# Kernel optimization log

Measured on AMD Instinct MI355X. Metric: run time of the kernel, lower is better.

## Reference

```python
import jax, jax.numpy as jnp
import numpy as np

B, S, D, H = 2, 2048, 1024, 16
DK = D // H
NEG = -65504.0  # matches torch masked_fill value in source


def setup_inputs() -> dict:
    key = jax.random.key(0)
    ks = jax.random.split(key, 5)
    scale = 1.0 / np.sqrt(D)
    return {
        "x": jax.random.normal(ks[0], (B, S, D), dtype=jnp.float32),
        "W_q": jax.random.normal(ks[1], (D, D), dtype=jnp.float32) * scale,
        "W_k": jax.random.normal(ks[2], (D, D), dtype=jnp.float32) * scale,
        "W_v": jax.random.normal(ks[3], (D, D), dtype=jnp.float32) * scale,
        "W_o": jax.random.normal(ks[4], (D, D), dtype=jnp.float32) * scale,
    }


def reference(x, W_q, W_k, W_v, W_o):
    b, s, d = x.shape
    # nn.Linear(x) = x @ W.T ; split heads -> [b, h, s, dk]
    def proj(W):
        return (x @ W.T).reshape(b, s, H, DK).transpose(0, 2, 1, 3)
    q, k, v = proj(W_q), proj(W_k), proj(W_v)
    scores = jnp.einsum("bhqd,bhkd->bhqk", q, k) / jnp.sqrt(jnp.float32(DK))
    causal = jnp.tril(jnp.ones((s, s), dtype=bool))  # True where attending allowed
    scores = jnp.where(causal, scores, NEG)
    attn = jax.nn.softmax(scores, axis=-1)  # attn_pdrop=0 -> dropout is identity
    out = jnp.einsum("bhqk,bhkd->bhqd", attn, v)
    out = out.transpose(0, 2, 1, 3).reshape(b, s, d)
    return out @ W_o.T
```

## Files before the change

### kernel.cpp

```cpp
#include <hip/hip_runtime.h>
#include <hip/hip_bf16.h>

typedef __attribute__((ext_vector_type(4))) float f32x4;
typedef __attribute__((ext_vector_type(8))) short bf16x8;

#define Bn 2
#define Sn 2048
#define Dn 1024
#define Hn 16
#define DKn 64
#define Mrows (Bn * Sn)

__device__ __forceinline__ unsigned short f2bf(float f) {
  unsigned int x = __float_as_uint(f);
  x += 0x7fffu + ((x >> 16) & 1u);
  return (unsigned short)(x >> 16);
}

__device__ __forceinline__ float bf2f(unsigned short u) {
  return __uint_as_float(((unsigned int)u) << 16);
}

__device__ __forceinline__ unsigned int cvtpk(float lo, float hi) {
  unsigned int r;
  asm("v_cvt_pk_bf16_f32 %0, %1, %2" : "=v"(r) : "v"(lo), "v"(hi));
  return r;
}

__device__ __forceinline__ float exp2a(float x) {
  float r;
  asm("v_exp_f32 %0, %1" : "=v"(r) : "v"(x));
  return r;
}

__device__ __forceinline__ f32x4 mfma16(bf16x8 a, bf16x8 b, f32x4 c) {
  return __builtin_amdgcn_mfma_f32_16x16x32_bf16(a, b, c, 0, 0, 0);
}

__device__ __forceinline__ f32x4 max4(f32x4 a, f32x4 b) {
  f32x4 r;
  r[0] = fmaxf(a[0], b[0]); r[1] = fmaxf(a[1], b[1]);
  r[2] = fmaxf(a[2], b[2]); r[3] = fmaxf(a[3], b[3]);
  return r;
}

__device__ __forceinline__ void gload_lds16(const unsigned short* g, unsigned short* l) {
  __builtin_amdgcn_global_load_lds(
      (const __attribute__((address_space(1))) void*)g,
      (__attribute__((address_space(3))) void*)l, 16, 0, 0);
}

__global__ __launch_bounds__(256)
void cvt_all(const float* __restrict__ x,  const float* __restrict__ wq,
             const float* __restrict__ wk, const float* __restrict__ wv,
             const float* __restrict__ wo,
             unsigned short* __restrict__ xb,  unsigned short* __restrict__ wqb,
             unsigned short* __restrict__ wkb, unsigned short* __restrict__ wvb,
             unsigned short* __restrict__ wob) {
  int i = (blockIdx.x * 256 + threadIdx.x) * 4;
  const float* src; unsigned short* dst; int off;
  int r = i >> 20;
  if (r < 4)       { src = x;  dst = xb;  off = i; }
  else if (r == 4) { src = wq; dst = wqb; off = i & 1048575; }
  else if (r == 5) { src = wk; dst = wkb; off = i & 1048575; }
  else if (r == 6) { src = wv; dst = wvb; off = i & 1048575; }
  else             { src = wo; dst = wob; off = i & 1048575; }
  float4 v = *(const float4*)(src + off);
  ushort4 o;
  o.x = f2bf(v.x); o.y = f2bf(v.y); o.z = f2bf(v.z); o.w = f2bf(v.w);
  *(ushort4*)(dst + off) = o;
}

template<int MODE>
__device__ __forceinline__ void gemm_body(const unsigned short* __restrict__ A,
                                          const unsigned short* __restrict__ W,
                                          unsigned short* __restrict__ Cb,
                                          float* __restrict__ Cf,
                                          unsigned short* As,
                                          unsigned short* Bs,
                                          int row0, int col0) {
  const int K = Dn, N = Dn;
  const int tid  = threadIdx.x;
  const int wid  = tid >> 6;
  const int lane = tid & 63;
  const int l15  = lane & 15;
  const int lg   = lane >> 4;
  const int wr = (wid >> 1) * 64;
  const int wc = (wid & 1) * 64;

  f32x4 acc[4][4] = {};

  const int lrow2 = lane >> 2;
  const int gs    = (lane & 3) ^ ((lane >> 3) & 3);
  const int swzr  = (l15 >> 1) & 3;

  auto stage = [&](int kt, int b) {
#pragma unroll
    for (int q = 0; q < 2; ++q) {
      int chunk = wid * 2 + q;
      int r = chunk * 16 + lrow2;
      gload_lds16(A + (size_t)(row0 + r) * K + kt + gs * 8,
                  &As[b * 4096 + chunk * 512]);
    }
#pragma unroll
    for (int q = 0; q < 2; ++q) {
      int chunk = wid * 2 + q;
      int r = chunk * 16 + lrow2;
      gload_lds16(W + (size_t)(col0 + r) * K + kt + gs * 8,
                  &Bs[b * 4096 + chunk * 512]);
    }
  };

  auto compute = [&](int b) {
    bf16x8 af[4], bfr[4];
#pragma unroll
    for (int m = 0; m < 4; ++m)
      af[m] = *(const bf16x8*)(&As[b * 4096 + (wr + m * 16 + l15) * 32 +
                                   ((lg ^ swzr) * 8)]);
#pragma unroll
    for (int n = 0; n < 4; ++n)
      bfr[n] = *(const bf16x8*)(&Bs[b * 4096 + (wc + n * 16 + l15) * 32 +
                                    ((lg ^ swzr) * 8)]);
    __builtin_amdgcn_s_setprio(1);
#pragma unroll
    for (int m = 0; m < 4; ++m)
#pragma unroll
      for (int n = 0; n < 4; ++n)
        acc[m][n] = mfma16(af[m], bfr[n], acc[m][n]);
    __builtin_amdgcn_s_setprio(0);
  };

  stage(0, 0);
  stage(32, 1);
  int cb = 0;
#pragma unroll 1
  for (int t = 0; t < 32; ++t) {
    if (t < 31) asm volatile("s_waitcnt vmcnt(4)" ::: "memory");
    else        asm volatile("s_waitcnt vmcnt(0)" ::: "memory");
    __builtin_amdgcn_sched_barrier(0);
    __builtin_amdgcn_s_barrier();
    __builtin_amdgcn_sched_barrier(0);
    if (t <= 29) {
      int sb = cb + 2; if (sb >= 3) sb -= 3;
      stage((t + 2) * 32, sb);
    }
    compute(cb);
    ++cb; if (cb == 3) cb = 0;
  }

#pragma unroll
  for (int m = 0; m < 4; ++m)
#pragma unroll
    for (int n = 0; n < 4; ++n) {
      int r0 = row0 + wr + m * 16 + lg * 4;
      int c  = col0 + wc + n * 16 + l15;
      if (MODE == 2) {
        int b = r0 >> 11, s = r0 & 2047;
        int h = c >> 6,  d = c & 63;
        ushort4 pw;
        pw.x = f2bf(acc[m][n][0]); pw.y = f2bf(acc[m][n][1]);
        pw.z = f2bf(acc[m][n][2]); pw.w = f2bf(acc[m][n][3]);
        *(ushort4*)(Cb + ((((size_t)b * Hn + h) * DKn + d) << 11) + s) = pw;
      } else {
#pragma unroll
        for (int j = 0; j < 4; ++j) {
          size_t idx = (size_t)(r0 + j) * N + c;
          float v = acc[m][n][j];
          if (MODE == 3)      Cf[idx] = v;
          else if (MODE == 0) Cb[idx] = f2bf(v * 0.18033688f);
          else                Cb[idx] = f2bf(v);
        }
      }
    }
}

__global__ __launch_bounds__(256, 3)
void gemm_qkv(const unsigned short* __restrict__ A,
              const unsigned short* __restrict__ W0,
              const unsigned short* __restrict__ W1,
              const unsigned short* __restrict__ W2,
              unsigned short* __restrict__ C0,
              unsigned short* __restrict__ C1,
              unsigned short* __restrict__ C2) {
  __shared__ unsigned short As[3 * 128 * 32];
  __shared__ unsigned short Bs[3 * 128 * 32];
  const int fid = blockIdx.x;
  const int panel = fid % 24;
  const int row0 = (fid / 24) * 128;
  const int col0 = (panel & 7) * 128;
  const int z = panel >> 3;
  if (z == 0)      gemm_body<0>(A, W0, C0, nullptr, As, Bs, row0, col0);
  else if (z == 1) gemm_body<1>(A, W1, C1, nullptr, As, Bs, row0, col0);
  else             gemm_body<2>(A, W2, C2, nullptr, As, Bs, row0, col0);
}

__global__ __launch_bounds__(256, 3)
void gemm_out(const unsigned short* __restrict__ A,
              const unsigned short* __restrict__ W,
              float* __restrict__ C) {
  __shared__ unsigned short As[3 * 128 * 32];
  __shared__ unsigned short Bs[3 * 128 * 32];
  gemm_body<3>(A, W, nullptr, C, As, Bs, blockIdx.x * 128, blockIdx.y * 128);
}

__global__ __launch_bounds__(512, 4)
void attn_part(const unsigned short* __restrict__ Qg,
               const unsigned short* __restrict__ Kg,
               const unsigned short* __restrict__ Vtg,
               unsigned short* __restrict__ Og,
               unsigned short* __restrict__ Pb,
               float* __restrict__ Pml) {
  const int bid = blockIdx.x;
  const int bh = bid & 31;
  const int j  = bid >> 5;
  const int bb = bh >> 4, hh = bh & 15;
  const int tid = threadIdx.x, wid = tid >> 6, lane = tid & 63;
  const int l15 = lane & 15, lg = lane >> 4;
  const int wq = wid * 16;
  const size_t baseQ = (size_t)bb * Sn * Dn + (size_t)hh * DKn;
  const size_t baseV = (size_t)bh * DKn * Sn;

  __shared__ unsigned short Ks[2][64 * 64];
  __shared__ unsigned short Vts[2][64 * 64];
  __shared__ unsigned short Ps[8][16 * 72];

  const int lrow  = lane >> 3;
  const int sgran = (lane & 7) ^ lrow;
  const int swz   = l15 & 7;

  const int g0 = 17 * j;
  int qt = 0;
  while ((qt + 1) * (qt + 2) <= g0) ++qt;
  int kt = g0 - qt * (qt + 1);

  int sqt = qt, skt = kt;
  auto stage = [&](int t, int b) {
    const int k0 = t << 6;
    gload_lds16(Kg + baseQ + (size_t)(k0 + wid * 8 + lrow) * Dn + sgran * 8,
                &Ks[b][wid * 512]);
    gload_lds16(Vtg + baseV + (size_t)(wid * 8 + lrow) * Sn + k0 + sgran * 8,
                &Vts[b][wid * 512]);
  };
  auto advs = [&]() { ++skt; if (skt == 2 * sqt + 2) { skt = 0; ++sqt; } };

  stage(skt, 0); advs();
  __syncthreads();

  bf16x8 qf[2];
  auto loadQ = [&](int qtile) {
    const int q0 = qtile * 128;
#pragma unroll
    for (int kd = 0; kd < 2; ++kd)
      qf[kd] = *(const bf16x8*)(Qg + baseQ +
               (size_t)(q0 + wq + l15) * Dn + kd * 32 + lg * 8);
  };
  loadQ(qt);

  f32x4 oacc[4] = {};
  float mrun = -1e30f;
  float lrun = 0.f;
  int pstart = kt;

  for (int i = 0; i < 17; ++i) {
    const int cur = i & 1;
    if (i < 16) { stage(skt, cur ^ 1); advs(); }
    const int k0 = kt << 6;
    const int q0 = qt * 128;

    if (k0 <= q0 + wq + 15) {
      f32x4 sf[4] = {};
      __builtin_amdgcn_s_setprio(1);
#pragma unroll
      for (int kn = 0; kn < 4; ++kn)
#pragma unroll
        for (int kd = 0; kd < 2; ++kd) {
          bf16x8 kf = *(const bf16x8*)(&Ks[cur][(kn * 16 + l15) * 64 +
                                              (((kd * 4 + lg) ^ swz) * 8)]);
          sf[kn] = mfma16(kf, qf[kd], sf[kn]);
        }
      __builtin_amdgcn_s_setprio(0);

      if (k0 + 63 > q0 + wq) {
        int qq = q0 + wq + l15;
#pragma unroll
        for (int kn = 0; kn < 4; ++kn)
#pragma unroll
          for (int jj = 0; jj < 4; ++jj) {
            int key = k0 + kn * 16 + lg * 4 + jj;
            if (key > qq) sf[kn][jj] = -1e30f;
          }
      }

      f32x4 mm = max4(max4(sf[0], sf[1]), max4(sf[2], sf[3]));
      float tl = fmaxf(fmaxf(mm[0], mm[1]), fmaxf(mm[2], mm[3]));
      if (__any(tl > mrun + 11.5f)) {
        float t = tl;
        t = fmaxf(t, __shfl_xor(t, 16));
        t = fmaxf(t, __shfl_xor(t, 32));
        float mnew = fmaxf(mrun, t);
        float corr = exp2a(mrun - mnew);
        mrun = mnew;
        lrun *= corr;
#pragma unroll
        for (int dn = 0; dn < 4; ++dn) oacc[dn] *= corr;
      }
      const float m = mrun;
#pragma unroll
      for (int kn = 0; kn < 4; ++kn) {
#pragma unroll
        for (int jj = 0; jj < 4; ++jj)
          sf[kn][jj] = exp2a(sf[kn][jj] - m);
        uint2 pw;
        pw.x = cvtpk(sf[kn][0], sf[kn][1]);
        pw.y = cvtpk(sf[kn][2], sf[kn][3]);
        *(uint2*)(&Ps[wid][l15 * 72 + kn * 16 + lg * 4]) = pw;
      }
      f32x4 sv = (sf[0] + sf[1]) + (sf[2] + sf[3]);
      lrun += (sv[0] + sv[1]) + (sv[2] + sv[3]);

      __builtin_amdgcn_s_setprio(1);
#pragma unroll
      for (int kk = 0; kk < 2; ++kk) {
        bf16x8 pf = *(const bf16x8*)(&Ps[wid][l15 * 72 + kk * 32 + lg * 8]);
#pragma unroll
        for (int dn = 0; dn < 4; ++dn) {
          bf16x8 vf = *(const bf16x8*)(&Vts[cur][(dn * 16 + l15) * 64 +
                                               (((kk * 4 + lg) ^ swz) * 8)]);
          oacc[dn] = mfma16(vf, pf, oacc[dn]);
        }
      }
      __builtin_amdgcn_s_setprio(0);
    }

    const bool segend = (kt == 2 * qt + 1);
    if (segend || i == 16) {
      if (pstart == 0 && segend) {
        float lt = lrun;
        lt += __shfl_xor(lt, 16);
        lt += __shfl_xor(lt, 32);
        float rinv = 1.0f / lt;
        int row = q0 + wq + l15;
#pragma unroll
        for (int dn = 0; dn < 4; ++dn) {
          ushort4 ow;
          ow.x = f2bf(oacc[dn][0] * rinv);
          ow.y = f2bf(oacc[dn][1] * rinv);
          ow.z = f2bf(oacc[dn][2] * rinv);
          ow.w = f2bf(oacc[dn][3] * rinv);
          *(ushort4*)(Og + baseQ + (size_t)row * Dn + dn * 16 + lg * 4) = ow;
        }
      } else {
        const int seg_s = qt * (qt + 1);
        const int ord = pstart ? ((seg_s + pstart) / 17 - seg_s / 17) : 0;
        const size_t slot = (size_t)((bh * 16 + qt) * 3 + ord);
        float lt = lrun;
        lt += __shfl_xor(lt, 16);
        lt += __shfl_xor(lt, 32);
        int rl = wq + l15;
#pragma unroll
        for (int dn = 0; dn < 4; ++dn) {
          ushort4 ow;
          ow.x = f2bf(oacc[dn][0]);
          ow.y = f2bf(oacc[dn][1]);
          ow.z = f2bf(oacc[dn][2]);
          ow.w = f2bf(oacc[dn][3]);
          *(ushort4*)(Pb + slot * 8192 + (size_t)rl * 64 + dn * 16 + lg * 4) = ow;
        }
        if (lg == 0) {
          Pml[slot * 256 + rl] = mrun;
          Pml[slot * 256 + 128 + rl] = lt;
        }
      }
      if (i < 16) {
        ++qt; kt = 0; pstart = 0;
        loadQ(qt);
        mrun = -1e30f; lrun = 0.f;
#pragma unroll
        for (int dn = 0; dn < 4; ++dn) oacc[dn] = f32x4{0.f, 0.f, 0.f, 0.f};
      }
    } else {
      ++kt;
    }
    __syncthreads();
  }
}

__global__ __launch_bounds__(256)
void attn_combine(const unsigned short* __restrict__ Pb,
                  const float* __restrict__ Pml,
                  unsigned short* __restrict__ Og) {
  const int b = blockIdx.x;
  const int bh = b >> 4, qt = b & 15;
  const int seg_s = qt * (qt + 1);
  const int seg_e = seg_s + 2 * qt + 2;
  const int c0 = (seg_s / 17 + 1) * 17;
  if (c0 >= seg_e) return;
  const int np = (c0 + 17 < seg_e) ? 3 : 2;
  const int bb = bh >> 4, hh = bh & 15;
  const size_t baseQ = (size_t)bb * Sn * Dn + (size_t)hh * DKn;
  const int q0 = qt * 128;
  const int slot0 = b * 3;
  const int r = threadIdx.x >> 1;
  const int c32 = (threadIdx.x & 1) * 32;

  float m0 = Pml[(size_t)slot0 * 256 + r];
  float l0 = Pml[(size_t)slot0 * 256 + 128 + r];
  float m1 = Pml[(size_t)(slot0 + 1) * 256 + r];
  float l1 = Pml[(size_t)(slot0 + 1) * 256 + 128 + r];
  float m2 = -1e30f, l2 = 0.f;
  if (np == 3) {
    m2 = Pml[(size_t)(slot0 + 2) * 256 + r];
    l2 = Pml[(size_t)(slot0 + 2) * 256 + 128 + r];
  }
  float M = fmaxf(fmaxf(m0, m1), m2);
  float w0 = exp2a(m0 - M), w1 = exp2a(m1 - M);
  float w2 = (np == 3) ? exp2a(m2 - M) : 0.f;
  float L = l0 * w0 + l1 * w1 + l2 * w2;

  float acc[32];
#pragma unroll
  for (int k = 0; k < 32; ++k) acc[k] = 0.f;

  auto accum = [&](int p, float w) {
    const unsigned short* src = Pb + (size_t)(slot0 + p) * 8192 + (size_t)r * 64 + c32;
#pragma unroll
    for (int k4 = 0; k4 < 8; ++k4) {
      ushort4 v = *(const ushort4*)(src + k4 * 4);
      acc[k4 * 4 + 0] += w * bf2f(v.x);
      acc[k4 * 4 + 1] += w * bf2f(v.y);
      acc[k4 * 4 + 2] += w * bf2f(v.z);
      acc[k4 * 4 + 3] += w * bf2f(v.w);
    }
  };
  accum(0, w0);
  accum(1, w1);
  if (np == 3) accum(2, w2);

  float rinv = 1.0f / L;
#pragma unroll
  for (int k4 = 0; k4 < 8; ++k4) {
    ushort4 o;
    o.x = f2bf(acc[k4 * 4 + 0] * rinv);
    o.y = f2bf(acc[k4 * 4 + 1] * rinv);
    o.z = f2bf(acc[k4 * 4 + 2] * rinv);
    o.w = f2bf(acc[k4 * 4 + 3] * rinv);
    *(ushort4*)(Og + baseQ + (size_t)(q0 + r) * Dn + c32 + k4 * 4) = o;
  }
}

extern "C" void kernel_launch(void* const* d_in, const int* in_sizes, int n_in,
                              void* d_out, int out_size, void* d_ws, size_t ws_size,
                              hipStream_t stream) {
  const float* x  = (const float*)d_in[0];
  const float* Wq = (const float*)d_in[1];
  const float* Wk = (const float*)d_in[2];
  const float* Wv = (const float*)d_in[3];
  const float* Wo = (const float*)d_in[4];
  float* out = (float*)d_out;

  char* ws = (char*)d_ws;
  size_t off = 0;
  unsigned short* xb  = (unsigned short*)(ws + off); off += (size_t)Mrows * Dn * 2;
  unsigned short* wqb = (unsigned short*)(ws + off); off += (size_t)Dn * Dn * 2;
  unsigned short* wkb = (unsigned short*)(ws + off); off += (size_t)Dn * Dn * 2;
  unsigned short* wvb = (unsigned short*)(ws + off); off += (size_t)Dn * Dn * 2;
  unsigned short* wob = (unsigned short*)(ws + off); off += (size_t)Dn * Dn * 2;
  unsigned short* Qb  = (unsigned short*)(ws + off); off += (size_t)Mrows * Dn * 2;
  unsigned short* Kb  = (unsigned short*)(ws + off); off += (size_t)Mrows * Dn * 2;
  unsigned short* Vtb = (unsigned short*)(ws + off); off += (size_t)Mrows * Dn * 2;
  unsigned short* Ob  = (unsigned short*)(ws + off); off += (size_t)Mrows * Dn * 2;
  unsigned short* Pb  = (unsigned short*)(ws + off); off += (size_t)1536 * 8192 * 2;
  float*          Pml = (float*)(ws + off);          off += (size_t)1536 * 256 * 4;

  cvt_all<<<8192, 256, 0, stream>>>(x, Wq, Wk, Wv, Wo, xb, wqb, wkb, wvb, wob);
  gemm_qkv<<<768, 256, 0, stream>>>(xb, wqb, wkb, wvb, Qb, Kb, Vtb);
  attn_part<<<512, 512, 0, stream>>>(Qb, Kb, Vtb, Ob, Pb, Pml);
  attn_combine<<<512, 256, 0, stream>>>(Pb, Pml, Ob);
  gemm_out<<<dim3(Mrows / 128, Dn / 128), 256, 0, stream>>>(Ob, wob, out);
}
```

Before: 109.8 us.

## Software-pipeline QK^T of next tile with softmax/PV of current tile

Restructures the attention loop so the QK^T MFMAs for the next key tile are issued before the softmax and PV work of the current tile, with ping-pong score registers. V gets a triple-buffered LDS slot and the prologue stages two tiles ahead, so one barrier per iteration replaces the old trailing syncthreads. The combine kernel's block-to-(bh,qt) mapping is also changed so consecutive blocks cover different heads. The intent is to overlap matrix-core work with exp/VALU work, at the cost of extra registers and LDS, which may lower occupancy.

```diff
diff --git a/kernel.cpp b/kernel.cpp
--- a/kernel.cpp
+++ b/kernel.cpp
@@ -221,7 +221,7 @@
   const size_t baseV = (size_t)bh * DKn * Sn;
 
   __shared__ unsigned short Ks[2][64 * 64];
-  __shared__ unsigned short Vts[2][64 * 64];
+  __shared__ unsigned short Vts[3][64 * 64];
   __shared__ unsigned short Ps[8][16 * 72];
 
   const int lrow  = lane >> 3;
@@ -229,22 +229,24 @@
   const int swz   = l15 & 7;
 
   const int g0 = 17 * j;
-  int qt = 0;
-  while ((qt + 1) * (qt + 2) <= g0) ++qt;
-  int kt = g0 - qt * (qt + 1);
-
-  int sqt = qt, skt = kt;
-  auto stage = [&](int t, int b) {
-    const int k0 = t << 6;
+  int qtC = 0;
+  while ((qtC + 1) * (qtC + 2) <= g0) ++qtC;
+  int ktC = g0 - qtC * (qtC + 1);
+  int qtN = qtC, ktN = ktC;
+  { ++ktN; if (ktN == 2 * qtN + 2) { ktN = 0; ++qtN; } }
+  int sqt = qtC, skt = ktC;
+  int snum = 0;
+
+  auto stage = [&]() {
+    const int k0 = skt << 6;
+    const int ksl = snum & 1, vsl = snum % 3;
     gload_lds16(Kg + baseQ + (size_t)(k0 + wid * 8 + lrow) * Dn + sgran * 8,
-                &Ks[b][wid * 512]);
+                &Ks[ksl][wid * 512]);
     gload_lds16(Vtg + baseV + (size_t)(wid * 8 + lrow) * Sn + k0 + sgran * 8,
-                &Vts[b][wid * 512]);
+                &Vts[vsl][wid * 512]);
+    ++snum;
+    ++skt; if (skt == 2 * sqt + 2) { skt = 0; ++sqt; }
   };
-  auto advs = [&]() { ++skt; if (skt == 2 * sqt + 2) { skt = 0; ++sqt; } };
-
-  stage(skt, 0); advs();
-  __syncthreads();
 
   bf16x8 qf[2];
   auto loadQ = [&](int qtile) {
@@ -254,44 +256,73 @@
       qf[kd] = *(const bf16x8*)(Qg + baseQ +
                (size_t)(q0 + wq + l15) * Dn + kd * 32 + lg * 8);
   };
-  loadQ(qt);
-
+
+  f32x4 sfA[4], sfB[4];
   f32x4 oacc[4] = {};
   float mrun = -1e30f;
   float lrun = 0.f;
-  int pstart = kt;
-
-  for (int i = 0; i < 17; ++i) {
-    const int cur = i & 1;
-    if (i < 16) { stage(skt, cur ^ 1); advs(); }
-    const int k0 = kt << 6;
-    const int q0 = qt * 128;
-
-    if (k0 <= q0 + wq + 15) {
-      f32x4 sf[4] = {};
-      __builtin_amdgcn_s_setprio(1);
-#pragma unroll
-      for (int kn = 0; kn < 4; ++kn)
-#pragma unroll
-        for (int kd = 0; kd < 2; ++kd) {
-          bf16x8 kf = *(const bf16x8*)(&Ks[cur][(kn * 16 + l15) * 64 +
-                                              (((kd * 4 + lg) ^ swz) * 8)]);
-          sf[kn] = mfma16(kf, qf[kd], sf[kn]);
-        }
-      __builtin_amdgcn_s_setprio(0);
-
-      if (k0 + 63 > q0 + wq) {
-        int qq = q0 + wq + l15;
+  int pstart = ktC;
+
+  stage(); stage();
+  loadQ(qtC);
+  asm volatile("s_waitcnt vmcnt(0)" ::: "memory");
+  __builtin_amdgcn_sched_barrier(0);
+  __builtin_amdgcn_s_barrier();
+  if ((ktC << 6) <= qtC * 128 + wq + 15) {
+#pragma unroll
+    for (int kn = 0; kn < 4; ++kn) sfA[kn] = f32x4{0.f, 0.f, 0.f, 0.f};
+    __builtin_amdgcn_s_setprio(1);
+#pragma unroll
+    for (int kn = 0; kn < 4; ++kn)
+#pragma unroll
+      for (int kd = 0; kd < 2; ++kd) {
+        bf16x8 kf = *(const bf16x8*)(&Ks[0][(kn * 16 + l15) * 64 +
+                                          (((kd * 4 + lg) ^ swz) * 8)]);
+        sfA[kn] = mfma16(kf, qf[kd], sfA[kn]);
+      }
+    __builtin_amdgcn_s_setprio(0);
+  }
+
+  auto body = [&](int i, f32x4 (&sfC)[4], f32x4 (&sfN)[4]) {
+    asm volatile("s_waitcnt vmcnt(0)" ::: "memory");
+    __builtin_amdgcn_sched_barrier(0);
+    __builtin_amdgcn_s_barrier();
+    if (i <= 14) stage();
+
+    if (i < 16) {
+      if (ktN == 0) loadQ(qtN);
+      const int k0n = ktN << 6;
+      if (k0n <= qtN * 128 + wq + 15) {
+        const int ksl = (i + 1) & 1;
+#pragma unroll
+        for (int kn = 0; kn < 4; ++kn) sfN[kn] = f32x4{0.f, 0.f, 0.f, 0.f};
+        __builtin_amdgcn_s_setprio(1);
 #pragma unroll
         for (int kn = 0; kn < 4; ++kn)
 #pragma unroll
+          for (int kd = 0; kd < 2; ++kd) {
+            bf16x8 kf = *(const bf16x8*)(&Ks[ksl][(kn * 16 + l15) * 64 +
+                                                 (((kd * 4 + lg) ^ swz) * 8)]);
+            sfN[kn] = mfma16(kf, qf[kd], sfN[kn]);
+          }
+        __builtin_amdgcn_s_setprio(0);
+      }
+    }
+
+    const int k0c = ktC << 6;
+    const int q0c = qtC * 128;
+    if (k0c <= q0c + wq + 15) {
+      if (k0c + 63 > q0c + wq) {
+        int qq = q0c + wq + l15;
+#pragma unroll
+        for (int kn = 0; kn < 4; ++kn)
+#pragma unroll
           for (int jj = 0; jj < 4; ++jj) {
-            int key = k0 + kn * 16 + lg * 4 + jj;
-            if (key > qq) sf[kn][jj] = -1e30f;
+            int key = k0c + kn * 16 + lg * 4 + jj;
+            if (key > qq) sfC[kn][jj] = -1e30f;
           }
       }
-
-      f32x4 mm = max4(max4(sf[0], sf[1]), max4(sf[2], sf[3]));
+      f32x4 mm = max4(max4(sfC[0], sfC[1]), max4(sfC[2], sfC[3]));
       float tl = fmaxf(fmaxf(mm[0], mm[1]), fmaxf(mm[2], mm[3]));
       if (__any(tl > mrun + 11.5f)) {
         float t = tl;
@@ -309,37 +340,38 @@
       for (int kn = 0; kn < 4; ++kn) {
 #pragma unroll
         for (int jj = 0; jj < 4; ++jj)
-          sf[kn][jj] = exp2a(sf[kn][jj] - m);
+          sfC[kn][jj] = exp2a(sfC[kn][jj] - m);
         uint2 pw;
-        pw.x = cvtpk(sf[kn][0], sf[kn][1]);
-        pw.y = cvtpk(sf[kn][2], sf[kn][3]);
+        pw.x = cvtpk(sfC[kn][0], sfC[kn][1]);
+        pw.y = cvtpk(sfC[kn][2], sfC[kn][3]);
         *(uint2*)(&Ps[wid][l15 * 72 + kn * 16 + lg * 4]) = pw;
       }
-      f32x4 sv = (sf[0] + sf[1]) + (sf[2] + sf[3]);
+      f32x4 sv = (sfC[0] + sfC[1]) + (sfC[2] + sfC[3]);
       lrun += (sv[0] + sv[1]) + (sv[2] + sv[3]);
 
+      const int vsl = i % 3;
       __builtin_amdgcn_s_setprio(1);
 #pragma unroll
       for (int kk = 0; kk < 2; ++kk) {
         bf16x8 pf = *(const bf16x8*)(&Ps[wid][l15 * 72 + kk * 32 + lg * 8]);
 #pragma unroll
         for (int dn = 0; dn < 4; ++dn) {
-          bf16x8 vf = *(const bf16x8*)(&Vts[cur][(dn * 16 + l15) * 64 +
-                                               (((kk * 4 + lg) ^ swz) * 8)]);
+          bf16x8 vf = *(const bf16x8*)(&Vts[vsl][(dn * 16 + l15) * 64 +
+                                                (((kk * 4 + lg) ^ swz) * 8)]);
           oacc[dn] = mfma16(vf, pf, oacc[dn]);
         }
       }
       __builtin_amdgcn_s_setprio(0);
     }
 
-    const bool segend = (kt == 2 * qt + 1);
+    const bool segend = (ktC == 2 * qtC + 1);
     if (segend || i == 16) {
       if (pstart == 0 && segend) {
         float lt = lrun;
         lt += __shfl_xor(lt, 16);
         lt += __shfl_xor(lt, 32);
         float rinv = 1.0f / lt;
-        int row = q0 + wq + l15;
+        int row = q0c + wq + l15;
 #pragma unroll
         for (int dn = 0; dn < 4; ++dn) {
           ushort4 ow;
@@ -350,9 +382,9 @@
           *(ushort4*)(Og + baseQ + (size_t)row * Dn + dn * 16 + lg * 4) = ow;
         }
       } else {
-        const int seg_s = qt * (qt + 1);
+        const int seg_s = qtC * (qtC + 1);
         const int ord = pstart ? ((seg_s + pstart) / 17 - seg_s / 17) : 0;
-        const size_t slot = (size_t)((bh * 16 + qt) * 3 + ord);
+        const size_t slot = (size_t)((bh * 16 + qtC) * 3 + ord);
         float lt = lrun;
         lt += __shfl_xor(lt, 16);
         lt += __shfl_xor(lt, 32);
@@ -372,16 +404,20 @@
         }
       }
       if (i < 16) {
-        ++qt; kt = 0; pstart = 0;
-        loadQ(qt);
+        pstart = 0;
         mrun = -1e30f; lrun = 0.f;
 #pragma unroll
         for (int dn = 0; dn < 4; ++dn) oacc[dn] = f32x4{0.f, 0.f, 0.f, 0.f};
       }
-    } else {
-      ++kt;
-    }
-    __syncthreads();
+    }
+    qtC = qtN; ktC = ktN;
+    ++ktN; if (ktN == 2 * qtN + 2) { ktN = 0; ++qtN; }
+  };
+
+#pragma unroll 1
+  for (int i = 0; i < 17; i += 2) {
+    body(i, sfA, sfB);
+    if (i + 1 < 17) body(i + 1, sfB, sfA);
   }
 }
 
@@ -389,8 +425,9 @@
 void attn_combine(const unsigned short* __restrict__ Pb,
                   const float* __restrict__ Pml,
                   unsigned short* __restrict__ Og) {
-  const int b = blockIdx.x;
-  const int bh = b >> 4, qt = b & 15;
+  const int bid = blockIdx.x;
+  const int qt = bid >> 5, bh = bid & 31;
+  const int b = bh * 16 + qt;
   const int seg_s = qt * (qt + 1);
   const int seg_e = seg_s + 2 * qt + 2;
   const int c0 = (seg_s / 17 + 1) * 17;
```

After: 109.2 us. No clear change (-0.5%).
